# Kernel optimization log

Measured on AMD Instinct MI355X. Metric: run time of the kernel, lower is better.

## Reference

```python
import jax, jax.numpy as jnp
import numpy as np

N, T, V, CIN, COUT = 64, 12, 256, 64, 64


def _conv1x1(h, w, b):
    # h: [n,c,v,w], w: [o,c] (1x1 conv kernel squeezed), b: [o]
    return jnp.einsum('ncvw,oc->novw', h, w) + b[None, :, None, None]


def setup_inputs() -> dict:
    key = jax.random.key(0)
    ks = jax.random.split(key, 8)
    x = jax.random.normal(ks[0], (N, CIN, T, V), jnp.float32)
    feats = jax.random.normal(ks[1], (N, 7, V, V), jnp.float32)
    mask = (jax.random.uniform(ks[2], (N, 1, V, V)) < 0.3).astype(jnp.float32)
    A = jnp.concatenate([feats, mask], axis=1)  # [N, 8, V, V]
    init = lambda k, shape, fan: jax.random.normal(k, shape, jnp.float32) / np.sqrt(fan).astype(np.float32)
    conv_w = init(ks[3], (COUT, CIN), CIN)
    conv_b = jnp.zeros((COUT,), jnp.float32)
    w1 = init(ks[4], (16, 7), 7)
    b1 = jnp.zeros((16,), jnp.float32)
    w2 = init(ks[5], (32, 16), 16)
    b2 = jnp.zeros((32,), jnp.float32)
    w3 = init(ks[6], (64, 32), 32)
    b3 = jnp.zeros((64,), jnp.float32)
    return dict(x=x, A=A, conv_w=conv_w, conv_b=conv_b,
                w1=w1, b1=b1, w2=w2, b2=b2, w3=w3, b3=b3)


def reference(x, A, conv_w, conv_b, w1, b1, w2, b2, w3, b3):
    # 1x1 temporal conv on node features: [n,cin,t,v] -> [n,cout,t,v]
    x = jnp.einsum('nctv,oc->notv', x, conv_w) + conv_b[None, :, None, None]
    mask = A[:, 7:]          # [n,1,v,v]
    h = A[:, :7]             # [n,7,v,v]
    # adjmatder MLP (dropout is identity at inference)
    h = jax.nn.relu(_conv1x1(h, w1, b1))
    h = jax.nn.relu(_conv1x1(h, w2, b2))
    h = jax.nn.relu(_conv1x1(h, w3, b3))   # [n,64,v,v]
    Aw = h * mask
    # per-channel graph convolution: [n,c,t,v] x [n,c,v,w] -> [n,c,t,w]
    out = jnp.einsum('nctv,ncvw->nctw', x, Aw)
    return out, Aw
```

## Files before the change

### kernel.cpp

```cpp
#include <hip/hip_runtime.h>
#include <hip/hip_bf16.h>

#define NB   64
#define TT   12
#define VV   256
#define CIN  64
#define COUT 64
#define VSQ  65536

typedef float f32x4 __attribute__((ext_vector_type(4)));

__global__ __launch_bounds__(256) void k1_conv(
    const float* __restrict__ x, const float* __restrict__ w,
    const float* __restrict__ b, float* __restrict__ y)
{
    const int nt = blockIdx.x;
    const int n  = nt / TT;
    const int t  = nt % TT;
    const int v  = threadIdx.x;

    const float* xp = x + ((long)n * CIN * TT + t) * VV + v;
    float xv[CIN];
    #pragma unroll 8
    for (int c = 0; c < CIN; ++c)
        xv[c] = xp[(long)c * TT * VV];

    float* yp = y + ((long)n * COUT * TT + t) * VV + v;

    for (int o0 = 0; o0 < COUT; o0 += 16) {
        float acc[16];
        #pragma unroll
        for (int i = 0; i < 16; ++i) acc[i] = b[o0 + i];
        #pragma unroll 8
        for (int c = 0; c < CIN; ++c) {
            const float xc = xv[c];
            #pragma unroll
            for (int i = 0; i < 16; ++i)
                acc[i] += w[(o0 + i) * CIN + c] * xc;
        }
        #pragma unroll
        for (int i = 0; i < 16; ++i)
            yp[(long)(o0 + i) * TT * VV] = acc[i];
    }
}

__global__ __launch_bounds__(256, 5) void k2_mlp(
    const float* __restrict__ A,
    const float* __restrict__ w1, const float* __restrict__ b1,
    const float* __restrict__ w2, const float* __restrict__ b2,
    const float* __restrict__ w3, const float* __restrict__ b3,
    float* __restrict__ Aw)
{
    const long idx = (long)blockIdx.x * 256 + threadIdx.x;
    const int  n   = (int)(idx >> 16);
    const int  rem = (int)(idx & (VSQ - 1));

    const float* ap = A + ((long)n * 8 << 16) + rem;
    float f[7];
    #pragma unroll
    for (int c = 0; c < 7; ++c) f[c] = ap[(long)c << 16];
    const float m = ap[(long)7 << 16];

    float h1[16];
    #pragma unroll
    for (int o = 0; o < 16; ++o) {
        float acc = b1[o];
        #pragma unroll
        for (int k = 0; k < 7; ++k) acc += w1[o * 7 + k] * f[k];
        h1[o] = fmaxf(acc, 0.f);
    }

    float h2[32];
    #pragma unroll
    for (int o = 0; o < 32; ++o) {
        float acc = b2[o];
        #pragma unroll
        for (int k = 0; k < 16; ++k) acc += w2[o * 16 + k] * h1[k];
        h2[o] = fmaxf(acc, 0.f);
    }

    float* op = Aw + ((long)n * COUT << 16) + rem;
    for (int o0 = 0; o0 < 64; o0 += 8) {
        float acc[8];
        #pragma unroll
        for (int i = 0; i < 8; ++i) acc[i] = b3[o0 + i];
        #pragma unroll
        for (int k = 0; k < 32; ++k) {
            #pragma unroll
            for (int i = 0; i < 8; ++i)
                acc[i] += w3[(o0 + i) * 32 + k] * h2[k];
        }
        #pragma unroll
        for (int i = 0; i < 8; ++i)
            __builtin_nontemporal_store(fmaxf(acc[i], 0.f) * m,
                                        op + ((long)(o0 + i) << 16));
    }
}

__global__ __launch_bounds__(256) void k3_einsum(
    const float* __restrict__ Aw, const float* __restrict__ y,
    float* __restrict__ out)
{
    __shared__ float ys[4][TT][VV];

    const int n   = blockIdx.x >> 4;
    const int c0  = (blockIdx.x & 15) * 4;
    const int tid = threadIdx.x;
    const int cq  = tid >> 6;
    const int w4  = (tid & 63) * 4;

    {
        const float* src = y + ((long)(n * COUT + c0) * TT) * VV;
        float* dst = &ys[0][0][0];
        #pragma unroll
        for (int it = 0; it < 12; ++it) {
            const int idx = tid + it * 256;
            *reinterpret_cast<float4*>(dst + idx * 4) =
                *reinterpret_cast<const float4*>(src + idx * 4);
        }
    }
    __syncthreads();

    const float* awp = Aw + (((long)(n * COUT + c0 + cq)) << 16) + w4;
    float4 acc[TT];
    #pragma unroll
    for (int t = 0; t < TT; ++t) acc[t] = make_float4(0.f, 0.f, 0.f, 0.f);

    for (int v0 = 0; v0 < VV; v0 += 4) {
        float4 xs[TT];
        #pragma unroll
        for (int t = 0; t < TT; ++t)
            xs[t] = *reinterpret_cast<const float4*>(&ys[cq][t][v0]);

        const f32x4 aw0 = __builtin_nontemporal_load(
            reinterpret_cast<const f32x4*>(awp + (long)(v0 + 0) * VV));
        const f32x4 aw1 = __builtin_nontemporal_load(
            reinterpret_cast<const f32x4*>(awp + (long)(v0 + 1) * VV));
        const f32x4 aw2 = __builtin_nontemporal_load(
            reinterpret_cast<const f32x4*>(awp + (long)(v0 + 2) * VV));
        const f32x4 aw3 = __builtin_nontemporal_load(
            reinterpret_cast<const f32x4*>(awp + (long)(v0 + 3) * VV));

        #pragma unroll
        for (int t = 0; t < TT; ++t) {
            acc[t].x += xs[t].x * aw0.x + xs[t].y * aw1.x + xs[t].z * aw2.x + xs[t].w * aw3.x;
            acc[t].y += xs[t].x * aw0.y + xs[t].y * aw1.y + xs[t].z * aw2.y + xs[t].w * aw3.y;
            acc[t].z += xs[t].x * aw0.z + xs[t].y * aw1.z + xs[t].z * aw2.z + xs[t].w * aw3.z;
            acc[t].w += xs[t].x * aw0.w + xs[t].y * aw1.w + xs[t].z * aw2.w + xs[t].w * aw3.w;
        }
    }

    float* op = out + ((long)(n * COUT + c0 + cq) * TT) * VV + w4;
    #pragma unroll
    for (int t = 0; t < TT; ++t)
        *reinterpret_cast<float4*>(op + t * VV) = acc[t];
}

extern "C" void kernel_launch(void* const* d_in, const int* in_sizes, int n_in,
                              void* d_out, int out_size, void* d_ws, size_t ws_size,
                              hipStream_t stream)
{
    const float* x      = (const float*)d_in[0];
    const float* A      = (const float*)d_in[1];
    const float* conv_w = (const float*)d_in[2];
    const float* conv_b = (const float*)d_in[3];
    const float* w1     = (const float*)d_in[4];
    const float* b1     = (const float*)d_in[5];
    const float* w2     = (const float*)d_in[6];
    const float* b2     = (const float*)d_in[7];
    const float* w3     = (const float*)d_in[8];
    const float* b3     = (const float*)d_in[9];

    float* out = (float*)d_out;
    float* Aw  = (float*)d_out + (long)NB * COUT * TT * VV;
    const size_t y_bytes = (size_t)NB * COUT * TT * VV * sizeof(float);

    float* y = (ws_size >= y_bytes) ? (float*)d_ws : out;

    k1_conv<<<NB * TT, 256, 0, stream>>>(x, conv_w, conv_b, y);

    k2_mlp<<<(NB * VSQ) / 256, 256, 0, stream>>>(A, w1, b1, w2, b2, w3, b3, Aw);

    k3_einsum<<<NB * (COUT / 4), 256, 0, stream>>>(Aw, y, out);
}
```

Before: 631.2 us.

## Fuse adjacency MLP with per-channel graph einsum through shared-memory tiles

Adds a fused kernel that computes the MLP-weighted adjacency for a 16x16 (v,w) tile across all 64 channels, writes it to the Aw output, and also stages it in swizzled LDS so the same block immediately does the graph-convolution einsum against y. This removes the re-read of the 64 MB Aw tensor from global memory in the separate einsum kernel. In exchange, each block runs 16 sequential MLP+sync phases with a large register footprint and lower parallelism (1024 blocks), and it rereads y from global or L2 for every tile. The old three-kernel path is kept as a fallback when the workspace is too small.

Result: slower. 770.0 us (+22.0%).

```diff
diff --git a/kernel.cpp b/kernel.cpp
--- a/kernel.cpp
+++ b/kernel.cpp
@@ -7,6 +7,8 @@
 #define CIN  64
 #define COUT 64
 #define VSQ  65536
+#define WT   16
+#define VC   16
 
 typedef float f32x4 __attribute__((ext_vector_type(4)));
 
@@ -42,6 +44,102 @@
         for (int i = 0; i < 16; ++i)
             yp[(long)(o0 + i) * TT * VV] = acc[i];
     }
+}
+
+__global__ __launch_bounds__(256) void k23_fused(
+    const float* __restrict__ A,
+    const float* __restrict__ w1, const float* __restrict__ b1,
+    const float* __restrict__ w2, const float* __restrict__ b2,
+    const float* __restrict__ w3, const float* __restrict__ b3,
+    const float* __restrict__ y,
+    float* __restrict__ Aw, float* __restrict__ out)
+{
+    __shared__ float awt[COUT * VC * WT];
+
+    const int n   = blockIdx.x >> 4;
+    const int w0  = (blockIdx.x & 15) * WT;
+    const int tid = threadIdx.x;
+
+    const int vj = tid >> 4;
+    const int wj = tid & 15;
+    const int cb = tid >> 2;
+    const int wg = tid & 3;
+
+    f32x4 acc[TT];
+    #pragma unroll
+    for (int t = 0; t < TT; ++t) acc[t] = (f32x4)(0.f);
+
+    const float* ybase  = y + ((long)(n * COUT + cb) * TT) * VV;
+    const float* Abase  = A + ((long)n * 8 << 16);
+    float*       awbase = Aw + ((long)n * COUT << 16);
+
+    for (int v0 = 0; v0 < VV; v0 += VC) {
+        const int pos = (v0 + vj) * VV + (w0 + wj);
+        const float* ap = Abase + pos;
+        float f[7];
+        #pragma unroll
+        for (int c = 0; c < 7; ++c) f[c] = ap[(long)c << 16];
+        const float m = ap[(long)7 << 16];
+
+        float h1[16];
+        #pragma unroll
+        for (int o = 0; o < 16; ++o) {
+            float s = b1[o];
+            #pragma unroll
+            for (int k = 0; k < 7; ++k) s += w1[o * 7 + k] * f[k];
+            h1[o] = fmaxf(s, 0.f);
+        }
+        float h2[32];
+        #pragma unroll
+        for (int o = 0; o < 32; ++o) {
+            float s = b2[o];
+            #pragma unroll
+            for (int k = 0; k < 16; ++k) s += w2[o * 16 + k] * h1[k];
+            h2[o] = fmaxf(s, 0.f);
+        }
+        for (int o0 = 0; o0 < 64; o0 += 16) {
+            float a16[16];
+            #pragma unroll
+            for (int i = 0; i < 16; ++i) a16[i] = b3[o0 + i];
+            #pragma unroll
+            for (int k = 0; k < 32; ++k) {
+                #pragma unroll
+                for (int i = 0; i < 16; ++i)
+                    a16[i] += w3[(o0 + i) * 32 + k] * h2[k];
+            }
+            #pragma unroll
+            for (int i = 0; i < 16; ++i) {
+                const int c = o0 + i;
+                const float av = fmaxf(a16[i], 0.f) * m;
+                __builtin_nontemporal_store(av, awbase + ((long)c << 16) + pos);
+                const int L = (c * (VC * WT) + vj * WT + wj) ^ ((c & 7) << 2);
+                awt[L] = av;
+            }
+        }
+        __syncthreads();
+
+        f32x4 awv[VC];
+        #pragma unroll
+        for (int vv = 0; vv < VC; ++vv) {
+            const int L = (cb * (VC * WT) + vv * WT + wg * 4) ^ ((cb & 7) << 2);
+            awv[vv] = *reinterpret_cast<const f32x4*>(&awt[L]);
+        }
+        #pragma unroll
+        for (int t = 0; t < TT; ++t) {
+            #pragma unroll
+            for (int q = 0; q < 4; ++q) {
+                const f32x4 yv = *reinterpret_cast<const f32x4*>(ybase + t * VV + v0 + q * 4);
+                acc[t] += yv.x * awv[q * 4 + 0] + yv.y * awv[q * 4 + 1]
+                        + yv.z * awv[q * 4 + 2] + yv.w * awv[q * 4 + 3];
+            }
+        }
+        __syncthreads();
+    }
+
+    float* obase = out + ((long)(n * COUT + cb) * TT) * VV + w0 + wg * 4;
+    #pragma unroll
+    for (int t = 0; t < TT; ++t)
+        __builtin_nontemporal_store(acc[t], reinterpret_cast<f32x4*>(obase + t * VV));
 }
 
 __global__ __launch_bounds__(256, 5) void k2_mlp(
@@ -69,7 +167,6 @@
         for (int k = 0; k < 7; ++k) acc += w1[o * 7 + k] * f[k];
         h1[o] = fmaxf(acc, 0.f);
     }
-
     float h2[32];
     #pragma unroll
     for (int o = 0; o < 32; ++o) {
@@ -78,7 +175,6 @@
         for (int k = 0; k < 16; ++k) acc += w2[o * 16 + k] * h1[k];
         h2[o] = fmaxf(acc, 0.f);
     }
-
     float* op = Aw + ((long)n * COUT << 16) + rem;
     for (int o0 = 0; o0 < 64; o0 += 8) {
         float acc[8];
@@ -175,11 +271,14 @@
     float* Aw  = (float*)d_out + (long)NB * COUT * TT * VV;
     const size_t y_bytes = (size_t)NB * COUT * TT * VV * sizeof(float);
 
-    float* y = (ws_size >= y_bytes) ? (float*)d_ws : out;
-
-    k1_conv<<<NB * TT, 256, 0, stream>>>(x, conv_w, conv_b, y);
-
-    k2_mlp<<<(NB * VSQ) / 256, 256, 0, stream>>>(A, w1, b1, w2, b2, w3, b3, Aw);
-
-    k3_einsum<<<NB * (COUT / 4), 256, 0, stream>>>(Aw, y, out);
-}
+    if (ws_size >= y_bytes) {
+        float* y = (float*)d_ws;
+        k1_conv<<<NB * TT, 256, 0, stream>>>(x, conv_w, conv_b, y);
+        k23_fused<<<NB * (VV / WT), 256, 0, stream>>>(
+            A, w1, b1, w2, b2, w3, b3, y, Aw, out);
+    } else {
+        k1_conv<<<NB * TT, 256, 0, stream>>>(x, conv_w, conv_b, out);
+        k2_mlp<<<(NB * VSQ) / 256, 256, 0, stream>>>(A, w1, b1, w2, b2, w3, b3, Aw);
+        k3_einsum<<<NB * (COUT / 4), 256, 0, stream>>>(Aw, out, out);
+    }
+}
```

## Restructure MLP third layer via shared-memory h2 tile and register-held weights

Applied to the files above, without the earlier changes.

The k2_mlp kernel now writes the second-layer activations and the mask for a block of 256 positions into shared memory. Each thread then keeps a 4x32 slice of w3 in registers and computes 4 output channels across 16 positions, using float4 shared loads and float4 nontemporal stores. This replaces per-thread scalar loads of w3 and scalar stores with reused weight registers and wider stores, which should lower instruction and load pressure. It adds a block barrier, about 34KB of shared memory, and removes the occupancy hint, so occupancy may change.

Result: slower. 668.1 us (+5.8%).

```diff
diff --git a/kernel.cpp b/kernel.cpp
--- a/kernel.cpp
+++ b/kernel.cpp
@@ -7,6 +7,7 @@
 #define CIN  64
 #define COUT 64
 #define VSQ  65536
+#define PP   256
 
 typedef float f32x4 __attribute__((ext_vector_type(4)));
 
@@ -44,56 +45,91 @@
     }
 }
 
-__global__ __launch_bounds__(256, 5) void k2_mlp(
+__global__ __launch_bounds__(256) void k2_mlp(
     const float* __restrict__ A,
     const float* __restrict__ w1, const float* __restrict__ b1,
     const float* __restrict__ w2, const float* __restrict__ b2,
     const float* __restrict__ w3, const float* __restrict__ b3,
     float* __restrict__ Aw)
 {
-    const long idx = (long)blockIdx.x * 256 + threadIdx.x;
-    const int  n   = (int)(idx >> 16);
-    const int  rem = (int)(idx & (VSQ - 1));
-
-    const float* ap = A + ((long)n * 8 << 16) + rem;
-    float f[7];
-    #pragma unroll
-    for (int c = 0; c < 7; ++c) f[c] = ap[(long)c << 16];
-    const float m = ap[(long)7 << 16];
-
-    float h1[16];
-    #pragma unroll
-    for (int o = 0; o < 16; ++o) {
-        float acc = b1[o];
-        #pragma unroll
-        for (int k = 0; k < 7; ++k) acc += w1[o * 7 + k] * f[k];
-        h1[o] = fmaxf(acc, 0.f);
-    }
-
-    float h2[32];
-    #pragma unroll
-    for (int o = 0; o < 32; ++o) {
-        float acc = b2[o];
-        #pragma unroll
-        for (int k = 0; k < 16; ++k) acc += w2[o * 16 + k] * h1[k];
-        h2[o] = fmaxf(acc, 0.f);
-    }
-
-    float* op = Aw + ((long)n * COUT << 16) + rem;
-    for (int o0 = 0; o0 < 64; o0 += 8) {
-        float acc[8];
-        #pragma unroll
-        for (int i = 0; i < 8; ++i) acc[i] = b3[o0 + i];
+    __shared__ float h2s[32][260];
+    __shared__ float ms[PP];
+
+    const int  tid  = threadIdx.x;
+    const long gpos = (long)blockIdx.x * PP;
+    const int  n    = (int)(gpos >> 16);
+    const int  rem0 = (int)(gpos & (VSQ - 1));
+
+    {
+        const float* ap = A + ((long)n * 8 << 16) + rem0 + tid;
+        float f[7];
+        #pragma unroll
+        for (int c = 0; c < 7; ++c) f[c] = ap[(long)c << 16];
+        ms[tid] = ap[(long)7 << 16];
+
+        float h1[16];
+        #pragma unroll
+        for (int o = 0; o < 16; ++o) {
+            float s = b1[o];
+            #pragma unroll
+            for (int k = 0; k < 7; ++k) s += w1[o * 7 + k] * f[k];
+            h1[o] = fmaxf(s, 0.f);
+        }
+        #pragma unroll
+        for (int o = 0; o < 32; ++o) {
+            float s = b2[o];
+            #pragma unroll
+            for (int k = 0; k < 16; ++k) s += w2[o * 16 + k] * h1[k];
+            h2s[o][tid] = fmaxf(s, 0.f);
+        }
+    }
+    __syncthreads();
+
+    const int cq = tid >> 4;
+    const int pl = tid & 15;
+
+    float w3r[4][32];
+    #pragma unroll
+    for (int i = 0; i < 4; ++i) {
+        #pragma unroll
+        for (int k4 = 0; k4 < 32; k4 += 4) {
+            const f32x4 wv = *reinterpret_cast<const f32x4*>(&w3[(cq * 4 + i) * 32 + k4]);
+            w3r[i][k4 + 0] = wv.x; w3r[i][k4 + 1] = wv.y;
+            w3r[i][k4 + 2] = wv.z; w3r[i][k4 + 3] = wv.w;
+        }
+    }
+    const float bb0 = b3[cq * 4 + 0], bb1 = b3[cq * 4 + 1];
+    const float bb2 = b3[cq * 4 + 2], bb3 = b3[cq * 4 + 3];
+
+    float* awbase = Aw + ((long)n * COUT << 16) + rem0;
+
+    #pragma unroll
+    for (int iter = 0; iter < 4; ++iter) {
+        const int q = pl + iter * 16;
+        f32x4 a0 = (f32x4)(bb0), a1 = (f32x4)(bb1);
+        f32x4 a2 = (f32x4)(bb2), a3 = (f32x4)(bb3);
         #pragma unroll
         for (int k = 0; k < 32; ++k) {
-            #pragma unroll
-            for (int i = 0; i < 8; ++i)
-                acc[i] += w3[(o0 + i) * 32 + k] * h2[k];
-        }
-        #pragma unroll
-        for (int i = 0; i < 8; ++i)
-            __builtin_nontemporal_store(fmaxf(acc[i], 0.f) * m,
-                                        op + ((long)(o0 + i) << 16));
+            const f32x4 h = *reinterpret_cast<const f32x4*>(&h2s[k][q * 4]);
+            a0 += w3r[0][k] * h;
+            a1 += w3r[1][k] * h;
+            a2 += w3r[2][k] * h;
+            a3 += w3r[3][k] * h;
+        }
+        const f32x4 m4 = *reinterpret_cast<const f32x4*>(&ms[q * 4]);
+        f32x4 r0, r1, r2, r3;
+        #pragma unroll
+        for (int j = 0; j < 4; ++j) {
+            r0[j] = fmaxf(a0[j], 0.f) * m4[j];
+            r1[j] = fmaxf(a1[j], 0.f) * m4[j];
+            r2[j] = fmaxf(a2[j], 0.f) * m4[j];
+            r3[j] = fmaxf(a3[j], 0.f) * m4[j];
+        }
+        const int pq = q * 4;
+        __builtin_nontemporal_store(r0, reinterpret_cast<f32x4*>(awbase + ((long)(cq * 4 + 0) << 16) + pq));
+        __builtin_nontemporal_store(r1, reinterpret_cast<f32x4*>(awbase + ((long)(cq * 4 + 1) << 16) + pq));
+        __builtin_nontemporal_store(r2, reinterpret_cast<f32x4*>(awbase + ((long)(cq * 4 + 2) << 16) + pq));
+        __builtin_nontemporal_store(r3, reinterpret_cast<f32x4*>(awbase + ((long)(cq * 4 + 3) << 16) + pq));
     }
 }
 
@@ -179,7 +215,7 @@
 
     k1_conv<<<NB * TT, 256, 0, stream>>>(x, conv_w, conv_b, y);
 
-    k2_mlp<<<(NB * VSQ) / 256, 256, 0, stream>>>(A, w1, b1, w2, b2, w3, b3, Aw);
+    k2_mlp<<<(NB * VSQ) / PP, 256, 0, stream>>>(A, w1, b1, w2, b2, w3, b3, Aw);
 
     k3_einsum<<<NB * (COUT / 4), 256, 0, stream>>>(Aw, y, out);
 }
```
